# Kernel tuning notes

Measured on AMD Instinct MI355X. Metric: run time of the kernel, lower is better.

The kernel has to match this reference:

```python
import jax, jax.numpy as jnp
import numpy as np

KERNEL = 3
PAD = (KERNEL - 1) // 2
KA = KERNEL * KERNEL          # kernel_area = 9
CENTER = KA // 2              # 4
CH_OUT = 64


def setup_inputs() -> dict:
    key = jax.random.key(0)
    k1, k2 = jax.random.split(key)
    x = jax.random.normal(k1, (8, 64, 128, 128), dtype=jnp.float32)
    weight = jax.random.uniform(k2, (1, 1, KA, 1, 1), dtype=jnp.float32)
    bias = jnp.zeros((1, 1, KA, 1, 1), dtype=jnp.float32)
    weight_center = jnp.ones((), dtype=jnp.float32)
    weight_median = jnp.ones((), dtype=jnp.float32)
    return {"x": x, "weight": weight, "bias": bias,
            "weight_center": weight_center, "weight_median": weight_median}


def _unfold_same(x):
    # x: (B, C, H, W) -> patches (B, C, KA, H, W), stride 1, zero pad
    B, C, H, W = x.shape
    xp = jnp.pad(x, ((0, 0), (0, 0), (PAD, PAD), (PAD, PAD)))
    # order matches F.unfold: index = ki*K + kj
    views = [xp[:, :, i:i + H, j:j + W] for i in range(KERNEL) for j in range(KERNEL)]
    return jnp.stack(views, axis=2)


def reference(x, weight, bias, weight_center, weight_median):
    B, C, H, W = x.shape
    x_sig = jax.nn.sigmoid(x)
    patches = _unfold_same(x_sig)                      # (B, C, KA, H, W)
    w = jax.nn.sigmoid(weight)
    b = jax.nn.sigmoid(bias)
    D = jnp.maximum(w, patches) + b                    # (B, C, KA, H, W)
    max_stat = jnp.sum(D, axis=2)
    # torch.median returns the lower middle element -> sort and index (KA-1)//2
    median_stat = jnp.sort(D, axis=2)[:, :, (KA - 1) // 2]
    mean_stat = jnp.mean(D, axis=2)
    center = patches[:, :, CENTER]
    out = (weight_center * center + weight_median * median_stat
           - max_stat - mean_stat)                     # (B, C, H, W)
    # expand to ch_out then sum over C_in -> every output channel is identical
    s = jnp.sum(out, axis=1)                           # (B, H, W)
    return jnp.broadcast_to(s[:, None], (B, CH_OUT, H, W))
```

## Files before the change

kernel.cpp:

```cpp
#include <hip/hip_runtime.h>

#define BATCH  8
#define CH     64
#define H      128
#define W      128
#define HW     (H * W)
#define RS     8
#define CPW    2
#define NCHUNK (CH / CPW)
#define NSTRIP (H / RS)

typedef float vfloat2 __attribute__((ext_vector_type(2)));
typedef float vfloat4 __attribute__((ext_vector_type(4)));

__device__ __forceinline__ float sigmoidf_(float v) {
    return 1.0f / (1.0f + __expf(-v));
}

__device__ __forceinline__ float pixel_val(
    const float p0, const float p1, const float p2,
    const float p3, const float p4, const float p5,
    const float p6, const float p7, const float p8,
    const float* __restrict__ wk, const float* __restrict__ bk,
    const float wc, const float wm)
{
    float d[9];
    d[0] = fmaxf(wk[0], p0) + bk[0];
    d[1] = fmaxf(wk[1], p1) + bk[1];
    d[2] = fmaxf(wk[2], p2) + bk[2];
    d[3] = fmaxf(wk[3], p3) + bk[3];
    d[4] = fmaxf(wk[4], p4) + bk[4];
    d[5] = fmaxf(wk[5], p5) + bk[5];
    d[6] = fmaxf(wk[6], p6) + bk[6];
    d[7] = fmaxf(wk[7], p7) + bk[7];
    d[8] = fmaxf(wk[8], p8) + bk[8];
    float sum = ((d[0] + d[1]) + (d[2] + d[3])) + ((d[5] + d[6]) + (d[7] + d[8])) + d[4];

    #define S2(a,bb) { float t = d[a]; d[a] = fminf(d[a], d[bb]); d[bb] = fmaxf(t, d[bb]); }
    S2(0,3) S2(1,4) S2(2,5) S2(0,1) S2(0,2) S2(4,5) S2(3,5)
    S2(1,2) S2(3,4) S2(1,3) S2(1,6) S2(4,6) S2(2,6)
    S2(2,3) S2(4,7) S2(2,4) S2(3,7)
    S2(4,8) S2(3,8) S2(3,4)
    #undef S2

    return wc * p4 + wm * d[4] - sum - sum * (1.0f / 9.0f);
}

__global__ __launch_bounds__(256) void partial_kernel(
    const float* __restrict__ x,
    const float* __restrict__ weight,
    const float* __restrict__ bias,
    const float* __restrict__ wcp,
    const float* __restrict__ wmp,
    float* __restrict__ ws)
{
    const int tid   = threadIdx.x;
    const int lane  = tid & 63;
    const int strip = blockIdx.x * 4 + (tid >> 6);
    const int chnk  = blockIdx.y;
    const int c0    = chnk * CPW;
    const int b     = blockIdx.z;

    const int row0 = strip * RS;
    const int col  = 2 * lane;

    float wk[9], bk[9];
    #pragma unroll
    for (int k = 0; k < 9; ++k) {
        wk[k] = sigmoidf_(weight[k]);
        bk[k] = sigmoidf_(bias[k]);
    }
    const float wc = wcp[0];
    const float wm = wmp[0];

    vfloat2 raw[CPW][RS + 2];
    #pragma unroll
    for (int cc = 0; cc < CPW; ++cc) {
        const float* base = x + ((size_t)b * CH + c0 + cc) * HW + col;
        #pragma unroll
        for (int rr = 0; rr < RS + 2; ++rr) {
            const int r_  = row0 + rr - 1;
            const int rcl = min(max(r_, 0), H - 1);
            raw[cc][rr] = *(const vfloat2*)(base + rcl * W);
        }
    }

    vfloat2 acc[RS];
    #pragma unroll
    for (int j = 0; j < RS; ++j) acc[j] = (vfloat2)(0.0f);

    #define SIGROW(cc, rr, Lr, Ar, Br, Rr)                                    \
    {                                                                         \
        const int  r_  = row0 + (rr) - 1;                                     \
        const bool okr = (r_ >= 0) & (r_ < H);                                \
        vfloat2 v = raw[cc][rr];                                              \
        Ar = okr ? sigmoidf_(v.x) : 0.0f;                                     \
        Br = okr ? sigmoidf_(v.y) : 0.0f;                                     \
        float lf = __shfl_up(Br, 1);                                          \
        float rg = __shfl_down(Ar, 1);                                        \
        Lr = (lane == 0)  ? 0.0f : lf;                                        \
        Rr = (lane == 63) ? 0.0f : rg;                                        \
    }

    #pragma unroll
    for (int cc = 0; cc < CPW; ++cc) {
        float L0, A0, B0, R0, L1, A1, B1, R1, L2, A2, B2, R2;
        SIGROW(cc, 0, L0, A0, B0, R0);
        SIGROW(cc, 1, L1, A1, B1, R1);

        #pragma unroll
        for (int j = 0; j < RS; ++j) {
            SIGROW(cc, j + 2, L2, A2, B2, R2);

            acc[j].x += pixel_val(L0, A0, B0,
                                  L1, A1, B1,
                                  L2, A2, B2, wk, bk, wc, wm);
            acc[j].y += pixel_val(A0, B0, R0,
                                  A1, B1, R1,
                                  A2, B2, R2, wk, bk, wc, wm);

            L0 = L1; A0 = A1; B0 = B1; R0 = R1;
            L1 = L2; A1 = A2; B1 = B2; R1 = R2;
        }
    }
    #undef SIGROW

    float* op = ws + ((size_t)b * NCHUNK + chnk) * HW + (size_t)row0 * W + col;
    #pragma unroll
    for (int j = 0; j < RS; ++j)
        *(vfloat2*)(op + (size_t)j * W) = acc[j];
}

__global__ __launch_bounds__(256) void broadcast_kernel(
    const float* __restrict__ ws,
    float* __restrict__ out)
{
    const int g  = (blockIdx.x * 256 + threadIdx.x) * 4;
    const int b  = g >> 14;
    const int p  = g & (HW - 1);
    const int c0 = blockIdx.y * 16;

    const float* wsb = ws + (size_t)b * NCHUNK * HW + p;
    vfloat4 s = (vfloat4)(0.0f);
    #pragma unroll
    for (int k = 0; k < NCHUNK; ++k)
        s += *(const vfloat4*)(wsb + (size_t)k * HW);

    float* base = out + ((size_t)b * CH + c0) * HW + p;
    #pragma unroll
    for (int j = 0; j < 16; ++j)
        __builtin_nontemporal_store(s, (vfloat4*)(base + (size_t)j * HW));
}

extern "C" void kernel_launch(void* const* d_in, const int* in_sizes, int n_in,
                              void* d_out, int out_size, void* d_ws, size_t ws_size,
                              hipStream_t stream) {
    const float* x      = (const float*)d_in[0];
    const float* weight = (const float*)d_in[1];
    const float* bias   = (const float*)d_in[2];
    const float* wcp    = (const float*)d_in[3];
    const float* wmp    = (const float*)d_in[4];
    float* out = (float*)d_out;
    float* ws  = (float*)d_ws;

    dim3 grid1(NSTRIP / 4, NCHUNK, BATCH);
    partial_kernel<<<grid1, 256, 0, stream>>>(x, weight, bias, wcp, wmp, ws);

    dim3 grid2(BATCH * HW / (4 * 256), CH / 16);
    broadcast_kernel<<<grid2, 256, 0, stream>>>(ws, out);
}
```

Baseline: 111.8 us.

## Fuse partial and broadcast kernels with LDS channel reduction and med3 median

Merges the two kernels into one. Each 1024-thread block handles a 4-row strip for all 64 channels of one batch: 16 waves each cover 4 channels and reduce their partials through shared memory, then broadcast the sums to the 64 output channels. This removes the workspace round trip and the second launch. The 20-comparator median network is replaced by a column-wise min/med3/max median-of-9 built on fmed3, and the uniform weights are pushed to scalar registers with readfirstlane. In exchange, grid parallelism drops to 256 large blocks, and the __syncthreads barriers may reduce overlap between the compute and store phases.

```diff
diff --git a/kernel.cpp b/kernel.cpp
--- a/kernel.cpp
+++ b/kernel.cpp
@@ -5,9 +5,9 @@
 #define H      128
 #define W      128
 #define HW     (H * W)
-#define RS     8
-#define CPW    2
-#define NCHUNK (CH / CPW)
+#define RS     4
+#define CPW    4
+#define NW     16
 #define NSTRIP (H / RS)
 
 typedef float vfloat2 __attribute__((ext_vector_type(2)));
@@ -17,61 +17,75 @@
     return 1.0f / (1.0f + __expf(-v));
 }
 
+__device__ __forceinline__ float uniformf_(float v) {
+    return __int_as_float(__builtin_amdgcn_readfirstlane(__float_as_int(v)));
+}
+
 __device__ __forceinline__ float pixel_val(
-    const float p0, const float p1, const float p2,
-    const float p3, const float p4, const float p5,
-    const float p6, const float p7, const float p8,
+    float c0t, float c0m, float c0b,
+    float c1t, float c1m, float c1b,
+    float c2t, float c2m, float c2b,
     const float* __restrict__ wk, const float* __restrict__ bk,
     const float wc, const float wm)
 {
-    float d[9];
-    d[0] = fmaxf(wk[0], p0) + bk[0];
-    d[1] = fmaxf(wk[1], p1) + bk[1];
-    d[2] = fmaxf(wk[2], p2) + bk[2];
-    d[3] = fmaxf(wk[3], p3) + bk[3];
-    d[4] = fmaxf(wk[4], p4) + bk[4];
-    d[5] = fmaxf(wk[5], p5) + bk[5];
-    d[6] = fmaxf(wk[6], p6) + bk[6];
-    d[7] = fmaxf(wk[7], p7) + bk[7];
-    d[8] = fmaxf(wk[8], p8) + bk[8];
-    float sum = ((d[0] + d[1]) + (d[2] + d[3])) + ((d[5] + d[6]) + (d[7] + d[8])) + d[4];
+    float a0 = fmaxf(wk[0], c0t) + bk[0];
+    float a1 = fmaxf(wk[3], c0m) + bk[3];
+    float a2 = fmaxf(wk[6], c0b) + bk[6];
+    float b0 = fmaxf(wk[1], c1t) + bk[1];
+    float b1 = fmaxf(wk[4], c1m) + bk[4];
+    float b2 = fmaxf(wk[7], c1b) + bk[7];
+    float e0 = fmaxf(wk[2], c2t) + bk[2];
+    float e1 = fmaxf(wk[5], c2m) + bk[5];
+    float e2 = fmaxf(wk[8], c2b) + bk[8];
 
-    #define S2(a,bb) { float t = d[a]; d[a] = fminf(d[a], d[bb]); d[bb] = fmaxf(t, d[bb]); }
-    S2(0,3) S2(1,4) S2(2,5) S2(0,1) S2(0,2) S2(4,5) S2(3,5)
-    S2(1,2) S2(3,4) S2(1,3) S2(1,6) S2(4,6) S2(2,6)
-    S2(2,3) S2(4,7) S2(2,4) S2(3,7)
-    S2(4,8) S2(3,8) S2(3,4)
-    #undef S2
+    float sum = ((a0 + b0) + (e0 + a1)) + ((e1 + a2) + (b2 + e2)) + b1;
 
-    return wc * p4 + wm * d[4] - sum - sum * (1.0f / 9.0f);
+    float mn0 = fminf(fminf(a0, a1), a2);
+    float md0 = __builtin_amdgcn_fmed3f(a0, a1, a2);
+    float mx0 = fmaxf(fmaxf(a0, a1), a2);
+    float mn1 = fminf(fminf(b0, b1), b2);
+    float md1 = __builtin_amdgcn_fmed3f(b0, b1, b2);
+    float mx1 = fmaxf(fmaxf(b0, b1), b2);
+    float mn2 = fminf(fminf(e0, e1), e2);
+    float md2 = __builtin_amdgcn_fmed3f(e0, e1, e2);
+    float mx2 = fmaxf(fmaxf(e0, e1), e2);
+
+    float lo  = fmaxf(fmaxf(mn0, mn1), mn2);
+    float mid = __builtin_amdgcn_fmed3f(md0, md1, md2);
+    float hi  = fminf(fminf(mx0, mx1), mx2);
+    float med = __builtin_amdgcn_fmed3f(lo, mid, hi);
+
+    return wc * c1m + wm * med - sum - sum * (1.0f / 9.0f);
 }
 
-__global__ __launch_bounds__(256) void partial_kernel(
+__global__ __launch_bounds__(1024) void fused_kernel(
     const float* __restrict__ x,
     const float* __restrict__ weight,
     const float* __restrict__ bias,
     const float* __restrict__ wcp,
     const float* __restrict__ wmp,
-    float* __restrict__ ws)
+    float* __restrict__ out)
 {
+    __shared__ float part[NW * RS * W];
+    __shared__ float tile[RS * W];
+
     const int tid   = threadIdx.x;
     const int lane  = tid & 63;
-    const int strip = blockIdx.x * 4 + (tid >> 6);
-    const int chnk  = blockIdx.y;
-    const int c0    = chnk * CPW;
-    const int b     = blockIdx.z;
-
-    const int row0 = strip * RS;
-    const int col  = 2 * lane;
+    const int wv    = tid >> 6;
+    const int strip = blockIdx.x;
+    const int b     = blockIdx.y;
+    const int c0    = wv * CPW;
+    const int row0  = strip * RS;
+    const int col   = 2 * lane;
 
     float wk[9], bk[9];
     #pragma unroll
     for (int k = 0; k < 9; ++k) {
-        wk[k] = sigmoidf_(weight[k]);
-        bk[k] = sigmoidf_(bias[k]);
+        wk[k] = uniformf_(sigmoidf_(weight[k]));
+        bk[k] = uniformf_(sigmoidf_(bias[k]));
     }
-    const float wc = wcp[0];
-    const float wm = wmp[0];
+    const float wc = uniformf_(wcp[0]);
+    const float wm = uniformf_(wmp[0]);
 
     vfloat2 raw[CPW][RS + 2];
     #pragma unroll
@@ -112,12 +126,10 @@
         for (int j = 0; j < RS; ++j) {
             SIGROW(cc, j + 2, L2, A2, B2, R2);
 
-            acc[j].x += pixel_val(L0, A0, B0,
-                                  L1, A1, B1,
-                                  L2, A2, B2, wk, bk, wc, wm);
-            acc[j].y += pixel_val(A0, B0, R0,
-                                  A1, B1, R1,
-                                  A2, B2, R2, wk, bk, wc, wm);
+            acc[j].x += pixel_val(L0, L1, L2,  A0, A1, A2,  B0, B1, B2,
+                                  wk, bk, wc, wm);
+            acc[j].y += pixel_val(A0, A1, A2,  B0, B1, B2,  R0, R1, R2,
+                                  wk, bk, wc, wm);
 
             L0 = L1; A0 = A1; B0 = B1; R0 = R1;
             L1 = L2; A1 = A2; B1 = B2; R1 = R2;
@@ -125,31 +137,29 @@
     }
     #undef SIGROW
 
-    float* op = ws + ((size_t)b * NCHUNK + chnk) * HW + (size_t)row0 * W + col;
     #pragma unroll
     for (int j = 0; j < RS; ++j)
-        *(vfloat2*)(op + (size_t)j * W) = acc[j];
-}
+        *(vfloat2*)&part[(wv * RS + j) * W + col] = acc[j];
+    __syncthreads();
 
-__global__ __launch_bounds__(256) void broadcast_kernel(
-    const float* __restrict__ ws,
-    float* __restrict__ out)
-{
-    const int g  = (blockIdx.x * 256 + threadIdx.x) * 4;
-    const int b  = g >> 14;
-    const int p  = g & (HW - 1);
-    const int c0 = blockIdx.y * 16;
+    if (tid < RS * W) {
+        float s = 0.0f;
+        #pragma unroll
+        for (int k = 0; k < NW; ++k)
+            s += part[k * (RS * W) + tid];
+        tile[tid] = s;
+    }
+    __syncthreads();
 
-    const float* wsb = ws + (size_t)b * NCHUNK * HW + p;
-    vfloat4 s = (vfloat4)(0.0f);
+    const int chunk = tid & 127;
+    const int g     = tid >> 7;
+    const int r     = chunk >> 5;
+    const int c4    = (chunk & 31) * 4;
+    const vfloat4 v = *(const vfloat4*)&tile[r * W + c4];
+    float* basep = out + ((size_t)b * CH + g) * HW + (size_t)(row0 + r) * W + c4;
     #pragma unroll
-    for (int k = 0; k < NCHUNK; ++k)
-        s += *(const vfloat4*)(wsb + (size_t)k * HW);
-
-    float* base = out + ((size_t)b * CH + c0) * HW + p;
-    #pragma unroll
-    for (int j = 0; j < 16; ++j)
-        __builtin_nontemporal_store(s, (vfloat4*)(base + (size_t)j * HW));
+    for (int j = 0; j < 8; ++j)
+        __builtin_nontemporal_store(v, (vfloat4*)(basep + (size_t)(8 * j) * HW));
 }
 
 extern "C" void kernel_launch(void* const* d_in, const int* in_sizes, int n_in,
@@ -161,11 +171,7 @@
     const float* wcp    = (const float*)d_in[3];
     const float* wmp    = (const float*)d_in[4];
     float* out = (float*)d_out;
-    float* ws  = (float*)d_ws;
 
-    dim3 grid1(NSTRIP / 4, NCHUNK, BATCH);
-    partial_kernel<<<grid1, 256, 0, stream>>>(x, weight, bias, wcp, wmp, ws);
-
-    dim3 grid2(BATCH * HW / (4 * 256), CH / 16);
-    broadcast_kernel<<<grid2, 256, 0, stream>>>(ws, out);
+    dim3 grid(NSTRIP, BATCH);
+    fused_kernel<<<grid, 1024, 0, stream>>>(x, weight, bias, wcp, wmp, out);
 }
```

Measured after the change: 115.9 us. +3.7%, slower.
